# Kernel optimization log

Hardware: AMD Instinct MI355X
Metric: run time of the kernel (lower is better)

The kernel has to match this reference:

```python
import jax, jax.numpy as jnp
import numpy as np

N_NODES = 100000
N_EDGES = 3200000
IN_C, HID, OUT_C = 128, 256, 128
N_GRAPHS = 64
EPS = 1e-5


def setup_inputs() -> dict:
    key = jax.random.key(0)
    ks = jax.random.split(key, 16)
    x = jax.random.normal(ks[0], (N_NODES, IN_C), dtype=jnp.float32)
    edge_index = jax.random.randint(ks[1], (2, N_EDGES), 0, N_NODES, dtype=jnp.int64 if jax.config.jax_enable_x64 else jnp.int32)
    batch = jnp.sort(jax.random.randint(ks[2], (N_NODES,), 0, N_GRAPHS, dtype=jnp.int32))
    def glorot(k, shape):
        lim = jnp.sqrt(6.0 / (shape[-2] + shape[-1]))
        return jax.random.uniform(k, shape, jnp.float32, -lim, lim)
    return {
        "x": x,
        "W_in": glorot(ks[3], (IN_C, HID)),
        "b_in": jnp.zeros((HID,), jnp.float32),
        "g_in": jnp.ones((HID,), jnp.float32),
        "be_in": jnp.zeros((HID,), jnp.float32),
        "W_hid": glorot(ks[4], (2, HID, HID)),
        "b_hid": jnp.zeros((2, HID), jnp.float32),
        "g_hid": jnp.ones((2, HID), jnp.float32),
        "be_hid": jnp.zeros((2, HID), jnp.float32),
        "W_out": glorot(ks[5], (HID, OUT_C)),
        "b_out": jnp.zeros((OUT_C,), jnp.float32),
        "g_out": jnp.ones((OUT_C,), jnp.float32),
        "be_out": jnp.zeros((OUT_C,), jnp.float32),
        "edge_index": edge_index,
        "batch": batch,
    }


def _gcn_norm(edge_index, n_nodes):
    # add self-loops, symmetric deg^-1/2 normalization (PyG GCNConv defaults)
    loop = jnp.arange(n_nodes, dtype=edge_index.dtype)
    src = jnp.concatenate([edge_index[0], loop])
    dst = jnp.concatenate([edge_index[1], loop])
    deg = jax.ops.segment_sum(jnp.ones_like(dst, dtype=jnp.float32), dst, num_segments=n_nodes)
    dinv = jnp.where(deg > 0, jax.lax.rsqrt(deg), 0.0)
    norm = dinv[src] * dinv[dst]  # [E+N]
    return src, dst, norm


def _block(x, W, b, g, be, src, dst, norm, n_nodes):
    h = x @ W  # [N, out]
    agg = jax.ops.segment_sum(h[src] * norm[:, None], dst, num_segments=n_nodes) + b
    a = jax.nn.leaky_relu(agg, negative_slope=0.01)
    mu = jnp.mean(a, axis=0)
    var = jnp.mean(jnp.square(a - mu), axis=0)
    return (a - mu) * jax.lax.rsqrt(var + EPS) * g + be


def reference(x, W_in, b_in, g_in, be_in, W_hid, b_hid, g_hid, be_hid,
              W_out, b_out, g_out, be_out, edge_index, batch):
    n = x.shape[0]
    src, dst, norm = _gcn_norm(edge_index, n)
    h = _block(x, W_in, b_in, g_in, be_in, src, dst, norm, n)
    for i in range(W_hid.shape[0]):
        h = _block(h, W_hid[i], b_hid[i], g_hid[i], be_hid[i], src, dst, norm, n)
    h = _block(h, W_out, b_out, g_out, be_out, src, dst, norm, n)
    # global mean pool over graphs
    sums = jax.ops.segment_sum(h, batch, num_segments=N_GRAPHS)
    cnts = jax.ops.segment_sum(jnp.ones((n,), h.dtype), batch, num_segments=N_GRAPHS)
    return sums / jnp.maximum(cnts, 1.0)[:, None]
```

## Files before the change

### kernel.cpp

```cpp
#include <hip/hip_runtime.h>
#include <stdint.h>

#define EPS_LN 1e-5f

typedef short bf16x8 __attribute__((ext_vector_type(8)));
typedef float f32x4  __attribute__((ext_vector_type(4)));

__device__ __forceinline__ unsigned short f2bf(float f) {
    unsigned u = __float_as_uint(f);
    unsigned r = (u + 0x7fffu + ((u >> 16) & 1u)) >> 16;
    return (unsigned short)r;
}
__device__ __forceinline__ float bf_lo(unsigned u) { return __uint_as_float(u << 16); }
__device__ __forceinline__ float bf_hi(unsigned u) { return __uint_as_float(u & 0xffff0000u); }

__device__ __forceinline__ void async16(void* lds, const void* g) {
    __builtin_amdgcn_global_load_lds(
        (const __attribute__((address_space(1))) unsigned int*)g,
        (__attribute__((address_space(3))) unsigned int*)lds, 16, 0, 0);
}


__global__ void count_deg_kernel(const int* __restrict__ dst, int E, unsigned* __restrict__ deg) {
    int e = blockIdx.x * blockDim.x + threadIdx.x;
    if (e < E) atomicAdd(&deg[dst[e]], 1u);
}

__global__ void block_sums_kernel(const unsigned* __restrict__ deg, unsigned* __restrict__ part, int N) {
    __shared__ unsigned s[256];
    int t = threadIdx.x;
    int i0 = blockIdx.x * 512 + t * 2;
    unsigned a = (i0 < N) ? deg[i0] : 0u;
    unsigned b = (i0 + 1 < N) ? deg[i0 + 1] : 0u;
    s[t] = a + b;
    __syncthreads();
    for (int off = 128; off > 0; off >>= 1) {
        if (t < off) s[t] += s[t + off];
        __syncthreads();
    }
    if (t == 0) part[blockIdx.x] = s[0];
}

__global__ void scan_part_kernel(unsigned* __restrict__ part, unsigned* __restrict__ row_ptr,
                                 int NB, int N) {
    __shared__ unsigned s[256];
    int t = threadIdx.x;
    unsigned v = (t < NB) ? part[t] : 0u;
    s[t] = v;
    __syncthreads();
    for (int off = 1; off < 256; off <<= 1) {
        unsigned u = (t >= off) ? s[t - off] : 0u;
        __syncthreads();
        s[t] += u;
        __syncthreads();
    }
    if (t < NB) part[t] = s[t] - v;
    if (t == 255) row_ptr[N] = s[255];
}

__global__ void scan_blocks_kernel(const unsigned* __restrict__ deg, const unsigned* __restrict__ part,
                                   unsigned* __restrict__ row_ptr, unsigned* __restrict__ cursor,
                                   float* __restrict__ dinv, int N) {
    __shared__ unsigned s[256];
    int t = threadIdx.x;
    int i0 = blockIdx.x * 512 + t * 2;
    unsigned a = (i0 < N) ? deg[i0] : 0u;
    unsigned b = (i0 + 1 < N) ? deg[i0 + 1] : 0u;
    unsigned pair = a + b;
    s[t] = pair;
    __syncthreads();
    for (int off = 1; off < 256; off <<= 1) {
        unsigned u = (t >= off) ? s[t - off] : 0u;
        __syncthreads();
        s[t] += u;
        __syncthreads();
    }
    unsigned excl = s[t] - pair + part[blockIdx.x];
    if (i0 < N) {
        row_ptr[i0] = excl; cursor[i0] = excl;
        dinv[i0] = rsqrtf((float)(a + 1u));
    }
    if (i0 + 1 < N) {
        row_ptr[i0 + 1] = excl + a; cursor[i0 + 1] = excl + a;
        dinv[i0 + 1] = rsqrtf((float)(b + 1u));
    }
}

__global__ void fill_csr_kernel(const int* __restrict__ src, const int* __restrict__ dst,
                                const float* __restrict__ dinv, int E,
                                unsigned* __restrict__ cursor, uint2* __restrict__ csr) {
    int e = blockIdx.x * blockDim.x + threadIdx.x;
    if (e < E) {
        int d = dst[e];
        int s = src[e];
        unsigned pos = atomicAdd(&cursor[d], 1u);
        float w = dinv[d] * dinv[s];
        csr[pos] = make_uint2((unsigned)s, __float_as_uint(w));
    }
}

__global__ void prep_all_kernel(const float* __restrict__ x, unsigned* __restrict__ xbf,
                                const float* __restrict__ W_in, unsigned short* __restrict__ Wt_in,
                                const float* __restrict__ W_hid, unsigned short* __restrict__ Wt_h0,
                                unsigned short* __restrict__ Wt_h1, int n2) {
    int i = blockIdx.x * blockDim.x + threadIdx.x;
    if (i < n2) {
        float2 v = *reinterpret_cast<const float2*>(&x[(size_t)i * 2]);
        xbf[i] = (unsigned)f2bf(v.x) | ((unsigned)f2bf(v.y) << 16);
        return;
    }
    int r = i - n2;
    if (r < 32768) {
        int k = r >> 8, c = r & 255;
        Wt_in[(size_t)c * 128 + k] = f2bf(W_in[r]);
    } else if (r < 32768 + 65536) {
        r -= 32768;
        int k = r >> 8, c = r & 255;
        Wt_h0[(size_t)c * 256 + k] = f2bf(W_hid[r]);
    } else if (r < 32768 + 131072) {
        r -= 32768 + 65536;
        int k = r >> 8, c = r & 255;
        Wt_h1[(size_t)c * 256 + k] = f2bf(W_hid[65536 + r]);
    }
}

template<int UPL, bool AFF, bool FINAL>
__global__ void aggregate_bf(const unsigned* __restrict__ X, void* __restrict__ outp,
                             const unsigned* __restrict__ row_ptr, const uint2* __restrict__ csr,
                             const float* __restrict__ dinv,
                             const float* __restrict__ ssum, const float* __restrict__ ssq,
                             const float* __restrict__ gg, const float* __restrict__ be, float invN,
                             const float* __restrict__ tW, const float* __restrict__ bias, int N) {
    constexpr int C = UPL * 64;
    constexpr unsigned RSU = C / 2;
    constexpr int PC = UPL * 2;

    __shared__ float sL[AFF ? C : 1], tL[AFF ? C : 1];
    if constexpr (AFF) {
        for (int i = threadIdx.x; i < C; i += 256) {
            float mu = ssum[i] * invN;
            float var = ssq[i] * invN - mu * mu;
            float s = gg[i] * rsqrtf(var + EPS_LN);
            sL[i] = s;
            tL[i] = be[i] - mu * s;
        }
        __syncthreads();
    }

    int node = blockIdx.x * 8 + (threadIdx.x >> 5);
    if (node >= N) return;
    int ll = threadIdx.x & 31;
    unsigned cu = (unsigned)ll * UPL;

    float di = dinv[node];
    float w0 = di * di;
    float acc[PC];
    float wsum = w0;
    {
        const unsigned* xr = X + (size_t)((unsigned)node * RSU + cu);
        if constexpr (UPL == 4) {
            uint4 v = *reinterpret_cast<const uint4*>(xr);
            unsigned uu[4] = {v.x, v.y, v.z, v.w};
            #pragma unroll
            for (int q = 0; q < 4; ++q) {
                acc[q * 2 + 0] = w0 * bf_lo(uu[q]);
                acc[q * 2 + 1] = w0 * bf_hi(uu[q]);
            }
        } else {
            uint2 v = *reinterpret_cast<const uint2*>(xr);
            acc[0] = w0 * bf_lo(v.x); acc[1] = w0 * bf_hi(v.x);
            acc[2] = w0 * bf_lo(v.y); acc[3] = w0 * bf_hi(v.y);
        }
    }
    unsigned e0 = row_ptr[node];
    unsigned e1 = row_ptr[node + 1];
    unsigned cnt = e1 - e0;
    unsigned full = cnt & ~7u;

    for (unsigned i = 0; i < full; i += 8) {
        uint2 p[8];
        #pragma unroll
        for (int u = 0; u < 8; ++u) p[u] = csr[e0 + i + u];
        if constexpr (UPL == 4) {
            uint4 v[8];
            #pragma unroll
            for (int u = 0; u < 8; ++u)
                v[u] = *reinterpret_cast<const uint4*>(X + (size_t)(p[u].x * RSU + cu));
            #pragma unroll
            for (int u = 0; u < 8; ++u) {
                float f = __uint_as_float(p[u].y);
                unsigned uu[4] = {v[u].x, v[u].y, v[u].z, v[u].w};
                #pragma unroll
                for (int q = 0; q < 4; ++q) {
                    acc[q * 2 + 0] += f * bf_lo(uu[q]);
                    acc[q * 2 + 1] += f * bf_hi(uu[q]);
                }
                wsum += f;
            }
        } else {
            uint2 v[8];
            #pragma unroll
            for (int u = 0; u < 8; ++u)
                v[u] = *reinterpret_cast<const uint2*>(X + (size_t)(p[u].x * RSU + cu));
            #pragma unroll
            for (int u = 0; u < 8; ++u) {
                float f = __uint_as_float(p[u].y);
                acc[0] += f * bf_lo(v[u].x); acc[1] += f * bf_hi(v[u].x);
                acc[2] += f * bf_lo(v[u].y); acc[3] += f * bf_hi(v[u].y);
                wsum += f;
            }
        }
    }
    for (unsigned i = full; i < cnt; ++i) {
        uint2 p = csr[e0 + i];
        float f = __uint_as_float(p.y);
        if constexpr (UPL == 4) {
            uint4 v = *reinterpret_cast<const uint4*>(X + (size_t)(p.x * RSU + cu));
            unsigned uu[4] = {v.x, v.y, v.z, v.w};
            #pragma unroll
            for (int q = 0; q < 4; ++q) {
                acc[q * 2 + 0] += f * bf_lo(uu[q]);
                acc[q * 2 + 1] += f * bf_hi(uu[q]);
            }
        } else {
            uint2 v = *reinterpret_cast<const uint2*>(X + (size_t)(p.x * RSU + cu));
            acc[0] += f * bf_lo(v.x); acc[1] += f * bf_hi(v.x);
            acc[2] += f * bf_lo(v.y); acc[3] += f * bf_hi(v.y);
        }
        wsum += f;
    }

    int col = ll * PC;
    float z[PC];
    #pragma unroll
    for (int j = 0; j < PC; ++j) {
        float f = acc[j];
        if constexpr (AFF) f = sL[col + j] * f + tL[col + j] * wsum;
        if constexpr (FINAL) {
            f = f + wsum * tW[col + j] + bias[col + j];
            f = f > 0.f ? f : 0.01f * f;
        }
        z[j] = f;
    }
    if constexpr (FINAL) {
        float* of = (float*)outp;
        *reinterpret_cast<float4*>(&of[(size_t)node * C + col]) = make_float4(z[0], z[1], z[2], z[3]);
    } else {
        unsigned* ou = (unsigned*)outp;
        if constexpr (UPL == 4) {
            uint4 pk;
            pk.x = (unsigned)f2bf(z[0]) | ((unsigned)f2bf(z[1]) << 16);
            pk.y = (unsigned)f2bf(z[2]) | ((unsigned)f2bf(z[3]) << 16);
            pk.z = (unsigned)f2bf(z[4]) | ((unsigned)f2bf(z[5]) << 16);
            pk.w = (unsigned)f2bf(z[6]) | ((unsigned)f2bf(z[7]) << 16);
            *reinterpret_cast<uint4*>(&ou[(size_t)((unsigned)node * RSU + cu)]) = pk;
        } else {
            uint2 pk;
            pk.x = (unsigned)f2bf(z[0]) | ((unsigned)f2bf(z[1]) << 16);
            pk.y = (unsigned)f2bf(z[2]) | ((unsigned)f2bf(z[3]) << 16);
            *reinterpret_cast<uint2*>(&ou[(size_t)((unsigned)node * RSU + cu)]) = pk;
        }
    }
}

template<int K, int NN, bool EPI>
__launch_bounds__(256)
__global__ void gemm_mfma(const unsigned short* __restrict__ Z, const unsigned short* __restrict__ Wt,
                          const float* __restrict__ bias, unsigned short* __restrict__ out,
                          float* __restrict__ stat_sum, float* __restrict__ stat_sq, int M) {
    __shared__ char smem[32768];
    __shared__ float csum[128], csq[128];

    const int tid = threadIdx.x;
    const int lane = tid & 63;
    const int w = tid >> 6;
    const int wr = (w >> 1) * 64;
    const int wc = (w & 1) * 64;
    const int rowBase = blockIdx.x * 128;
    const int colBase = blockIdx.y * 128;
    const int frow = lane & 15;
    const int kgrp = lane >> 4;

    f32x4 acc[4][4] = {};

    for (int kt = 0; kt < K / 64; ++kt) {
        #pragma unroll
        for (int i = 0; i < 4; ++i) {
            int g = (i * 4 + w) * 64 + lane;
            int r = g >> 3;
            int bl = (g & 7) * 16;
            int bg = bl ^ ((r & 7) << 4);
            const char* src = (const char*)Z + (((size_t)(rowBase + r) * K + kt * 64) << 1) + bg;
            async16(&smem[(i * 4 + w) * 1024], src);
        }
        #pragma unroll
        for (int i = 0; i < 4; ++i) {
            int g = (i * 4 + w) * 64 + lane;
            int r = g >> 3;
            int bl = (g & 7) * 16;
            int bg = bl ^ ((r & 7) << 4);
            const char* src = (const char*)Wt + (((size_t)(colBase + r) * K + kt * 64) << 1) + bg;
            async16(&smem[16384 + (i * 4 + w) * 1024], src);
        }
        __syncthreads();
        #pragma unroll
        for (int kk = 0; kk < 2; ++kk) {
            const int kbyte = kk * 64 + kgrp * 16;
            bf16x8 af[4], bfr[4];
            #pragma unroll
            for (int m = 0; m < 4; ++m) {
                int r = wr + m * 16 + frow;
                af[m] = *reinterpret_cast<const bf16x8*>(&smem[r * 128 + (kbyte ^ ((r & 7) << 4))]);
            }
            #pragma unroll
            for (int n = 0; n < 4; ++n) {
                int c = wc + n * 16 + frow;
                bfr[n] = *reinterpret_cast<const bf16x8*>(&smem[16384 + c * 128 + (kbyte ^ ((c & 7) << 4))]);
            }
            #pragma unroll
            for (int m = 0; m < 4; ++m)
                #pragma unroll
                for (int n = 0; n < 4; ++n)
                    acc[m][n] = __builtin_amdgcn_mfma_f32_16x16x32_bf16(bfr[n], af[m], acc[m][n], 0, 0, 0);
        }
        __syncthreads();
    }

    if constexpr (EPI) {
        if (tid < 128) { csum[tid] = 0.f; csq[tid] = 0.f; }
        __syncthreads();
    }

    #pragma unroll
    for (int n = 0; n < 4; ++n) {
        const int c_local = wc + n * 16 + kgrp * 4;
        const int col = colBase + c_local;
        float4 b4 = make_float4(0.f, 0.f, 0.f, 0.f);
        if constexpr (EPI) b4 = *reinterpret_cast<const float4*>(&bias[col]);
        float ps[4] = {0.f, 0.f, 0.f, 0.f}, pq[4] = {0.f, 0.f, 0.f, 0.f};
        #pragma unroll
        for (int m = 0; m < 4; ++m) {
            int row = rowBase + wr + m * 16 + frow;
            if (row < M) {
                float f0 = acc[m][n][0] + b4.x;
                float f1 = acc[m][n][1] + b4.y;
                float f2 = acc[m][n][2] + b4.z;
                float f3 = acc[m][n][3] + b4.w;
                if constexpr (EPI) {
                    f0 = f0 > 0.f ? f0 : 0.01f * f0;
                    f1 = f1 > 0.f ? f1 : 0.01f * f1;
                    f2 = f2 > 0.f ? f2 : 0.01f * f2;
                    f3 = f3 > 0.f ? f3 : 0.01f * f3;
                }
                uint2 pk;
                pk.x = (unsigned)f2bf(f0) | ((unsigned)f2bf(f1) << 16);
                pk.y = (unsigned)f2bf(f2) | ((unsigned)f2bf(f3) << 16);
                *reinterpret_cast<uint2*>(&out[(size_t)row * NN + col]) = pk;
                if constexpr (EPI) {
                    ps[0] += f0; ps[1] += f1; ps[2] += f2; ps[3] += f3;
                    pq[0] += f0 * f0; pq[1] += f1 * f1; pq[2] += f2 * f2; pq[3] += f3 * f3;
                }
            }
        }
        if constexpr (EPI) {
            #pragma unroll
            for (int s = 1; s < 16; s <<= 1) {
                #pragma unroll
                for (int j = 0; j < 4; ++j) {
                    ps[j] += __shfl_xor(ps[j], s);
                    pq[j] += __shfl_xor(pq[j], s);
                }
            }
            if (frow == 0) {
                #pragma unroll
                for (int j = 0; j < 4; ++j) {
                    atomicAdd(&csum[c_local + j], ps[j]);
                    atomicAdd(&csq[c_local + j], pq[j]);
                }
            }
        }
    }
    if constexpr (EPI) {
        __syncthreads();
        if (tid < 128) {
            atomicAdd(&stat_sum[colBase + tid], csum[tid]);
            atomicAdd(&stat_sq[colBase + tid], csq[tid]);
        }
    }
}

__global__ void prep_wout_tw(const float* __restrict__ W,
                             const float* __restrict__ ssum, const float* __restrict__ ssq,
                             const float* __restrict__ gg, const float* __restrict__ be, float invN,
                             unsigned short* __restrict__ Wt, float* __restrict__ tW) {
    if (blockIdx.x < 128) {
        int idx = blockIdx.x * 256 + threadIdx.x;
        int k = idx >> 7, c = idx & 127;
        float mu = ssum[k] * invN;
        float var = ssq[k] * invN - mu * mu;
        float s = gg[k] * rsqrtf(var + EPS_LN);
        Wt[(size_t)c * 256 + k] = f2bf(s * W[idx]);
    } else {
        int c = threadIdx.x;
        if (c < 128) {
            float acc = 0.f;
            for (int k = 0; k < 256; ++k) {
                float mu = ssum[k] * invN;
                float var = ssq[k] * invN - mu * mu;
                float s = gg[k] * rsqrtf(var + EPS_LN);
                float t = be[k] - mu * s;
                acc += t * W[k * 128 + c];
            }
            tW[c] = acc;
        }
    }
}

__global__ void stats_pool_kernel(const float* __restrict__ A, const int* __restrict__ batch,
                                  float* __restrict__ stat_sum, float* __restrict__ stat_sq,
                                  float* __restrict__ psums, float* __restrict__ pcnt, int N) {
    int c = threadIdx.x;
    int n0 = blockIdx.x * 256;
    if (n0 >= N) return;
    int n1 = min(n0 + 256, N);
    float cs = 0.f, cq = 0.f;
    float acc = 0.f, cacc = 0.f;
    int curg = -1;
    for (int n = n0; n < n1; ++n) {
        float v = A[(size_t)n * 128 + c];
        cs += v; cq += v * v;
        int g = batch[n];
        if (g != curg) {
            if (curg >= 0) {
                atomicAdd(&psums[curg * 128 + c], acc);
                if (c == 0) atomicAdd(&pcnt[curg], cacc);
            }
            acc = 0.f; cacc = 0.f; curg = g;
        }
        acc += v;
        cacc += 1.f;
    }
    if (curg >= 0) {
        atomicAdd(&psums[curg * 128 + c], acc);
        if (c == 0) atomicAdd(&pcnt[curg], cacc);
    }
    atomicAdd(&stat_sum[c], cs);
    atomicAdd(&stat_sq[c], cq);
}

__global__ void divide_kernel(const float* __restrict__ psums, const float* __restrict__ pcnt,
                              const float* __restrict__ ssum, const float* __restrict__ ssq,
                              const float* __restrict__ gg, const float* __restrict__ be, float invN,
                              float* __restrict__ out) {
    int i = blockIdx.x * blockDim.x + threadIdx.x;
    if (i < 64 * 128) {
        int g = i >> 7, c = i & 127;
        float mu = ssum[c] * invN;
        float var = ssq[c] * invN - mu * mu;
        float s = gg[c] * rsqrtf(var + EPS_LN);
        float t = be[c] - mu * s;
        float cnt = pcnt[g];
        out[i] = (cnt > 0.f) ? s * (psums[i] / cnt) + t : 0.f;
    }
}

extern "C" void kernel_launch(void* const* d_in, const int* in_sizes, int n_in,
                              void* d_out, int out_size, void* d_ws, size_t ws_size,
                              hipStream_t stream) {
    const float* x      = (const float*)d_in[0];
    const float* W_in   = (const float*)d_in[1];
    const float* b_in   = (const float*)d_in[2];
    const float* g_in   = (const float*)d_in[3];
    const float* be_in  = (const float*)d_in[4];
    const float* W_hid  = (const float*)d_in[5];
    const float* b_hid  = (const float*)d_in[6];
    const float* g_hid  = (const float*)d_in[7];
    const float* be_hid = (const float*)d_in[8];
    const float* W_out  = (const float*)d_in[9];
    const float* b_out  = (const float*)d_in[10];
    const float* g_out  = (const float*)d_in[11];
    const float* be_out = (const float*)d_in[12];
    const int*   eidx   = (const int*)d_in[13];
    const int*   batch  = (const int*)d_in[14];
    float* out = (float*)d_out;

    const int N = in_sizes[14];
    const int E = in_sizes[13] / 2;
    const int Npad = ((N + 127) / 128) * 128;
    const int NB = (N + 511) / 512;
    const int* e_src = eidx;
    const int* e_dst = eidx + E;

    char* ws = (char*)d_ws;
    size_t off = 0;
    auto alloc = [&](size_t bytes) -> void* {
        void* p = ws + off;
        off = (off + bytes + 255) & ~(size_t)255;
        return p;
    };
    char* B1 = (char*)alloc((size_t)Npad * 256 * 2);
    char* B2 = (char*)alloc((size_t)Npad * 256 * 2);
    unsigned* deg      = (unsigned*)alloc((size_t)N * 4);
    float*    dinv     = (float*)alloc((size_t)N * 4);
    unsigned* row_ptr  = (unsigned*)alloc((size_t)(N + 1) * 4);
    unsigned* cursor   = (unsigned*)alloc((size_t)N * 4);
    unsigned* part     = (unsigned*)alloc(256 * 4);
    uint2*    csr      = (uint2*)alloc((size_t)E * 8);
    unsigned short* Wt_in  = (unsigned short*)alloc(256 * 128 * 2);
    unsigned short* Wt_h0  = (unsigned short*)alloc(256 * 256 * 2);
    unsigned short* Wt_h1  = (unsigned short*)alloc(256 * 256 * 2);
    unsigned short* Wt_out = (unsigned short*)alloc(128 * 256 * 2);
    float*    tW       = (float*)alloc(128 * 4);
    float*    stats    = (float*)alloc(4 * 512 * 4);
    float*    psums    = (float*)alloc(64 * 128 * 4);
    float*    pcnt     = (float*)alloc(64 * 4);

    float* s1 = stats + 0 * 512, *q1 = s1 + 256;
    float* s2 = stats + 1 * 512, *q2 = s2 + 256;
    float* s3 = stats + 2 * 512, *q3 = s3 + 256;
    float* s4 = stats + 3 * 512, *q4 = s4 + 256;

    const float invN = 1.0f / (float)N;

    hipMemsetAsync(deg, 0, (size_t)N * 4, stream);
    hipMemsetAsync(stats, 0, ((char*)pcnt + 64 * 4) - (char*)stats, stream);

    int egrid = (E + 255) / 256;
    count_deg_kernel<<<egrid, 256, 0, stream>>>(e_dst, E, deg);
    block_sums_kernel<<<NB, 256, 0, stream>>>(deg, part, N);
    scan_part_kernel<<<1, 256, 0, stream>>>(part, row_ptr, NB, N);
    scan_blocks_kernel<<<NB, 256, 0, stream>>>(deg, part, row_ptr, cursor, dinv, N);
    fill_csr_kernel<<<egrid, 256, 0, stream>>>(e_src, e_dst, dinv, E, cursor, csr);

    {
        int total = N * 64 + 32768 + 65536 + 65536;
        prep_all_kernel<<<(total + 255) / 256, 256, 0, stream>>>(
            x, (unsigned*)B2, W_in, Wt_in, W_hid, Wt_h0, Wt_h1, N * 64);
    }

    const int aggGrid = (N + 7) / 8;
    dim3 gg256(Npad / 128, 2);

    aggregate_bf<2, false, false><<<aggGrid, 256, 0, stream>>>(
        (const unsigned*)B2, B1, row_ptr, csr, dinv,
        nullptr, nullptr, nullptr, nullptr, invN, nullptr, nullptr, N);
    gemm_mfma<128, 256, true><<<gg256, 256, 0, stream>>>(
        (const unsigned short*)B1, Wt_in, b_in, (unsigned short*)B2, s1, q1, N);

    aggregate_bf<4, true, false><<<aggGrid, 256, 0, stream>>>(
        (const unsigned*)B2, B1, row_ptr, csr, dinv,
        s1, q1, g_in, be_in, invN, nullptr, nullptr, N);
    gemm_mfma<256, 256, true><<<gg256, 256, 0, stream>>>(
        (const unsigned short*)B1, Wt_h0, b_hid, (unsigned short*)B2, s2, q2, N);

    aggregate_bf<4, true, false><<<aggGrid, 256, 0, stream>>>(
        (const unsigned*)B2, B1, row_ptr, csr, dinv,
        s2, q2, g_hid, be_hid, invN, nullptr, nullptr, N);
    gemm_mfma<256, 256, true><<<gg256, 256, 0, stream>>>(
        (const unsigned short*)B1, Wt_h1, b_hid + 256, (unsigned short*)B2, s3, q3, N);

    prep_wout_tw<<<129, 256, 0, stream>>>(W_out, s3, q3, g_hid + 256, be_hid + 256, invN, Wt_out, tW);
    gemm_mfma<256, 128, false><<<dim3(Npad / 128, 1), 256, 0, stream>>>(
        (const unsigned short*)B2, Wt_out, nullptr, (unsigned short*)B1, nullptr, nullptr, N);
    aggregate_bf<2, false, true><<<aggGrid, 256, 0, stream>>>(
        (const unsigned*)B1, B2, row_ptr, csr, dinv,
        nullptr, nullptr, nullptr, nullptr, invN, tW, b_out, N);

    stats_pool_kernel<<<(N + 255) / 256, 128, 0, stream>>>(
        (const float*)B2, batch, s4, q4, psums, pcnt, N);
    divide_kernel<<<(64 * 128 + 255) / 256, 256, 0, stream>>>(
        psums, pcnt, s4, q4, g_out, be_out, invN, out);
}
```

Before: 1.314 ms.

## Fuse neighbor aggregation with MFMA GEMM and stats epilogue per 16-row tile

```diff
diff --git a/kernel.cpp b/kernel.cpp
--- a/kernel.cpp
+++ b/kernel.cpp
@@ -124,28 +124,228 @@
     }
 }
 
+template<int K, int NN, bool AFF>
+__launch_bounds__(512, 4)
+__global__ void fused_aggemm(const unsigned* __restrict__ X, const unsigned short* __restrict__ Wt,
+                             const float* __restrict__ bias,
+                             const float* __restrict__ ssum, const float* __restrict__ ssq,
+                             const float* __restrict__ gg, const float* __restrict__ be, float invN,
+                             unsigned short* __restrict__ out,
+                             const unsigned* __restrict__ row_ptr, const uint2* __restrict__ csr,
+                             const float* __restrict__ dinv,
+                             float* __restrict__ stat_sum, float* __restrict__ stat_sq, int N) {
+    constexpr int UPL = K / 64;
+    constexpr int PC  = UPL * 2;
+    constexpr unsigned RSU = K / 2;
+
+    __shared__ char atile[16 * K * 2];
+    __shared__ float sL[AFF ? K : 1], tL[AFF ? K : 1];
+    __shared__ float csum[NN], csq[NN];
+
+    const int tid = threadIdx.x;
+
+    if constexpr (AFF) {
+        for (int i = tid; i < K; i += 512) {
+            float mu = ssum[i] * invN;
+            float var = ssq[i] * invN - mu * mu;
+            float s = gg[i] * rsqrtf(var + EPS_LN);
+            sL[i] = s; tL[i] = be[i] - mu * s;
+        }
+    }
+    for (int i = tid; i < NN; i += 512) { csum[i] = 0.f; csq[i] = 0.f; }
+    __syncthreads();
+
+    const int rrow = tid >> 5;
+    const int ll = tid & 31;
+    const int node = blockIdx.x * 16 + rrow;
+    const unsigned cu = (unsigned)ll * UPL;
+
+    float acc[PC];
+    #pragma unroll
+    for (int j = 0; j < PC; ++j) acc[j] = 0.f;
+    float wsum = 0.f;
+
+    if (node < N) {
+        float di = dinv[node];
+        float w0 = di * di;
+        wsum = w0;
+        {
+            const unsigned* xr = X + (size_t)((unsigned)node * RSU + cu);
+            if constexpr (UPL == 4) {
+                uint4 v = *reinterpret_cast<const uint4*>(xr);
+                unsigned uu[4] = {v.x, v.y, v.z, v.w};
+                #pragma unroll
+                for (int q = 0; q < 4; ++q) {
+                    acc[q * 2 + 0] = w0 * bf_lo(uu[q]);
+                    acc[q * 2 + 1] = w0 * bf_hi(uu[q]);
+                }
+            } else {
+                uint2 v = *reinterpret_cast<const uint2*>(xr);
+                acc[0] = w0 * bf_lo(v.x); acc[1] = w0 * bf_hi(v.x);
+                acc[2] = w0 * bf_lo(v.y); acc[3] = w0 * bf_hi(v.y);
+            }
+        }
+        unsigned e0 = row_ptr[node];
+        unsigned e1 = row_ptr[node + 1];
+        unsigned cnt = e1 - e0;
+        unsigned full = cnt & ~7u;
+
+        for (unsigned i = 0; i < full; i += 8) {
+            uint2 p[8];
+            #pragma unroll
+            for (int u = 0; u < 8; ++u) p[u] = csr[e0 + i + u];
+            if constexpr (UPL == 4) {
+                uint4 v[8];
+                #pragma unroll
+                for (int u = 0; u < 8; ++u)
+                    v[u] = *reinterpret_cast<const uint4*>(X + (size_t)(p[u].x * RSU + cu));
+                #pragma unroll
+                for (int u = 0; u < 8; ++u) {
+                    float f = __uint_as_float(p[u].y);
+                    unsigned uu[4] = {v[u].x, v[u].y, v[u].z, v[u].w};
+                    #pragma unroll
+                    for (int q = 0; q < 4; ++q) {
+                        acc[q * 2 + 0] += f * bf_lo(uu[q]);
+                        acc[q * 2 + 1] += f * bf_hi(uu[q]);
+                    }
+                    wsum += f;
+                }
+            } else {
+                uint2 v[8];
+                #pragma unroll
+                for (int u = 0; u < 8; ++u)
+                    v[u] = *reinterpret_cast<const uint2*>(X + (size_t)(p[u].x * RSU + cu));
+                #pragma unroll
+                for (int u = 0; u < 8; ++u) {
+                    float f = __uint_as_float(p[u].y);
+                    acc[0] += f * bf_lo(v[u].x); acc[1] += f * bf_hi(v[u].x);
+                    acc[2] += f * bf_lo(v[u].y); acc[3] += f * bf_hi(v[u].y);
+                    wsum += f;
+                }
+            }
+        }
+        for (unsigned i = full; i < cnt; ++i) {
+            uint2 p = csr[e0 + i];
+            float f = __uint_as_float(p.y);
+            if constexpr (UPL == 4) {
+                uint4 v = *reinterpret_cast<const uint4*>(X + (size_t)(p.x * RSU + cu));
+                unsigned uu[4] = {v.x, v.y, v.z, v.w};
+                #pragma unroll
+                for (int q = 0; q < 4; ++q) {
+                    acc[q * 2 + 0] += f * bf_lo(uu[q]);
+                    acc[q * 2 + 1] += f * bf_hi(uu[q]);
+                }
+            } else {
+                uint2 v = *reinterpret_cast<const uint2*>(X + (size_t)(p.x * RSU + cu));
+                acc[0] += f * bf_lo(v.x); acc[1] += f * bf_hi(v.x);
+                acc[2] += f * bf_lo(v.y); acc[3] += f * bf_hi(v.y);
+            }
+            wsum += f;
+        }
+
+        if constexpr (AFF) {
+            int col = ll * PC;
+            #pragma unroll
+            for (int j = 0; j < PC; ++j)
+                acc[j] = sL[col + j] * acc[j] + tL[col + j] * wsum;
+        }
+    }
+
+    {
+        char* myrow = atile + rrow * (K * 2);
+        if constexpr (UPL == 4) {
+            uint4 pk;
+            pk.x = (unsigned)f2bf(acc[0]) | ((unsigned)f2bf(acc[1]) << 16);
+            pk.y = (unsigned)f2bf(acc[2]) | ((unsigned)f2bf(acc[3]) << 16);
+            pk.z = (unsigned)f2bf(acc[4]) | ((unsigned)f2bf(acc[5]) << 16);
+            pk.w = (unsigned)f2bf(acc[6]) | ((unsigned)f2bf(acc[7]) << 16);
+            int off = (ll * 16) ^ ((rrow & 7) << 4);
+            *reinterpret_cast<uint4*>(myrow + off) = pk;
+        } else {
+            uint2 pk;
+            pk.x = (unsigned)f2bf(acc[0]) | ((unsigned)f2bf(acc[1]) << 16);
+            pk.y = (unsigned)f2bf(acc[2]) | ((unsigned)f2bf(acc[3]) << 16);
+            int off = (ll * 8) ^ ((rrow & 7) << 4);
+            *reinterpret_cast<uint2*>(myrow + off) = pk;
+        }
+    }
+    __syncthreads();
+
+    const int w = tid >> 6;
+    const int lane = tid & 63;
+    const int frow = lane & 15;
+    const int kgrp = lane >> 4;
+    f32x4 macc[2] = {};
+
+    #pragma unroll
+    for (int kt = 0; kt < K / 32; ++kt) {
+        int aoff = frow * (K * 2) + ((kt * 64 + kgrp * 16) ^ ((frow & 7) << 4));
+        bf16x8 af = *reinterpret_cast<const bf16x8*>(atile + aoff);
+        #pragma unroll
+        for (int n = 0; n < 2; ++n) {
+            int c = w * 32 + n * 16 + frow;
+            bf16x8 bfr = *reinterpret_cast<const bf16x8*>(Wt + (size_t)c * K + kt * 32 + kgrp * 8);
+            macc[n] = __builtin_amdgcn_mfma_f32_16x16x32_bf16(bfr, af, macc[n], 0, 0, 0);
+        }
+    }
+
+    const int orow = blockIdx.x * 16 + frow;
+    const bool rok = orow < N;
+    #pragma unroll
+    for (int n = 0; n < 2; ++n) {
+        const int c0 = w * 32 + n * 16 + kgrp * 4;
+        float4 b4 = *reinterpret_cast<const float4*>(&bias[c0]);
+        float f0 = macc[n][0] + b4.x;
+        float f1 = macc[n][1] + b4.y;
+        float f2 = macc[n][2] + b4.z;
+        float f3 = macc[n][3] + b4.w;
+        f0 = f0 > 0.f ? f0 : 0.01f * f0;
+        f1 = f1 > 0.f ? f1 : 0.01f * f1;
+        f2 = f2 > 0.f ? f2 : 0.01f * f2;
+        f3 = f3 > 0.f ? f3 : 0.01f * f3;
+        float ps[4], pq[4];
+        if (rok) {
+            uint2 pk;
+            pk.x = (unsigned)f2bf(f0) | ((unsigned)f2bf(f1) << 16);
+            pk.y = (unsigned)f2bf(f2) | ((unsigned)f2bf(f3) << 16);
+            *reinterpret_cast<uint2*>(&out[(size_t)orow * NN + c0]) = pk;
+            ps[0] = f0; ps[1] = f1; ps[2] = f2; ps[3] = f3;
+            pq[0] = f0 * f0; pq[1] = f1 * f1; pq[2] = f2 * f2; pq[3] = f3 * f3;
+        } else {
+            ps[0] = ps[1] = ps[2] = ps[3] = 0.f;
+            pq[0] = pq[1] = pq[2] = pq[3] = 0.f;
+        }
+        #pragma unroll
+        for (int s = 1; s < 16; s <<= 1) {
+            #pragma unroll
+            for (int j = 0; j < 4; ++j) {
+                ps[j] += __shfl_xor(ps[j], s);
+                pq[j] += __shfl_xor(pq[j], s);
+            }
+        }
+        if (frow == 0) {
+            #pragma unroll
+            for (int j = 0; j < 4; ++j) {
+                atomicAdd(&csum[c0 + j], ps[j]);
+                atomicAdd(&csq[c0 + j], pq[j]);
+            }
+        }
+    }
+    __syncthreads();
+    for (int i = tid; i < NN; i += 512) {
+        atomicAdd(&stat_sum[i], csum[i]);
+        atomicAdd(&stat_sq[i], csq[i]);
+    }
+}
+
 template<int UPL, bool AFF, bool FINAL>
 __global__ void aggregate_bf(const unsigned* __restrict__ X, void* __restrict__ outp,
                              const unsigned* __restrict__ row_ptr, const uint2* __restrict__ csr,
                              const float* __restrict__ dinv,
-                             const float* __restrict__ ssum, const float* __restrict__ ssq,
-                             const float* __restrict__ gg, const float* __restrict__ be, float invN,
                              const float* __restrict__ tW, const float* __restrict__ bias, int N) {
     constexpr int C = UPL * 64;
     constexpr unsigned RSU = C / 2;
     constexpr int PC = UPL * 2;
-
-    __shared__ float sL[AFF ? C : 1], tL[AFF ? C : 1];
-    if constexpr (AFF) {
-        for (int i = threadIdx.x; i < C; i += 256) {
-            float mu = ssum[i] * invN;
-            float var = ssq[i] * invN - mu * mu;
-            float s = gg[i] * rsqrtf(var + EPS_LN);
-            sL[i] = s;
-            tL[i] = be[i] - mu * s;
-        }
-        __syncthreads();
-    }
 
     int node = blockIdx.x * 8 + (threadIdx.x >> 5);
     if (node >= N) return;
@@ -158,19 +358,9 @@
     float wsum = w0;
     {
         const unsigned* xr = X + (size_t)((unsigned)node * RSU + cu);
-        if constexpr (UPL == 4) {
-            uint4 v = *reinterpret_cast<const uint4*>(xr);
-            unsigned uu[4] = {v.x, v.y, v.z, v.w};
-            #pragma unroll
-            for (int q = 0; q < 4; ++q) {
-                acc[q * 2 + 0] = w0 * bf_lo(uu[q]);
-                acc[q * 2 + 1] = w0 * bf_hi(uu[q]);
-            }
-        } else {
-            uint2 v = *reinterpret_cast<const uint2*>(xr);
-            acc[0] = w0 * bf_lo(v.x); acc[1] = w0 * bf_hi(v.x);
-            acc[2] = w0 * bf_lo(v.y); acc[3] = w0 * bf_hi(v.y);
-        }
+        uint2 v = *reinterpret_cast<const uint2*>(xr);
+        acc[0] = w0 * bf_lo(v.x); acc[1] = w0 * bf_hi(v.x);
+        acc[2] = w0 * bf_lo(v.y); acc[3] = w0 * bf_hi(v.y);
     }
     unsigned e0 = row_ptr[node];
     unsigned e1 = row_ptr[node + 1];
@@ -181,52 +371,24 @@
         uint2 p[8];
         #pragma unroll
         for (int u = 0; u < 8; ++u) p[u] = csr[e0 + i + u];
-        if constexpr (UPL == 4) {
-            uint4 v[8];
-            #pragma unroll
-            for (int u = 0; u < 8; ++u)
-                v[u] = *reinterpret_cast<const uint4*>(X + (size_t)(p[u].x * RSU + cu));
-            #pragma unroll
-            for (int u = 0; u < 8; ++u) {
-                float f = __uint_as_float(p[u].y);
-                unsigned uu[4] = {v[u].x, v[u].y, v[u].z, v[u].w};
-                #pragma unroll
-                for (int q = 0; q < 4; ++q) {
-                    acc[q * 2 + 0] += f * bf_lo(uu[q]);
-                    acc[q * 2 + 1] += f * bf_hi(uu[q]);
-                }
-                wsum += f;
-            }
-        } else {
-            uint2 v[8];
-            #pragma unroll
-            for (int u = 0; u < 8; ++u)
-                v[u] = *reinterpret_cast<const uint2*>(X + (size_t)(p[u].x * RSU + cu));
-            #pragma unroll
-            for (int u = 0; u < 8; ++u) {
-                float f = __uint_as_float(p[u].y);
-                acc[0] += f * bf_lo(v[u].x); acc[1] += f * bf_hi(v[u].x);
-                acc[2] += f * bf_lo(v[u].y); acc[3] += f * bf_hi(v[u].y);
-                wsum += f;
-            }
+        uint2 v[8];
+        #pragma unroll
+        for (int u = 0; u < 8; ++u)
+            v[u] = *reinterpret_cast<const uint2*>(X + (size_t)(p[u].x * RSU + cu));
+        #pragma unroll
+        for (int u = 0; u < 8; ++u) {
+            float f = __uint_as_float(p[u].y);
+            acc[0] += f * bf_lo(v[u].x); acc[1] += f * bf_hi(v[u].x);
+            acc[2] += f * bf_lo(v[u].y); acc[3] += f * bf_hi(v[u].y);
+            wsum += f;
         }
     }
     for (unsigned i = full; i < cnt; ++i) {
         uint2 p = csr[e0 + i];
+        uint2 v = *reinterpret_cast<const uint2*>(X + (size_t)(p.x * RSU + cu));
         float f = __uint_as_float(p.y);
-        if constexpr (UPL == 4) {
-            uint4 v = *reinterpret_cast<const uint4*>(X + (size_t)(p.x * RSU + cu));
-            unsigned uu[4] = {v.x, v.y, v.z, v.w};
-            #pragma unroll
-            for (int q = 0; q < 4; ++q) {
-                acc[q * 2 + 0] += f * bf_lo(uu[q]);
-                acc[q * 2 + 1] += f * bf_hi(uu[q]);
-            }
-        } else {
-            uint2 v = *reinterpret_cast<const uint2*>(X + (size_t)(p.x * RSU + cu));
-            acc[0] += f * bf_lo(v.x); acc[1] += f * bf_hi(v.x);
-            acc[2] += f * bf_lo(v.y); acc[3] += f * bf_hi(v.y);
-        }
+        acc[0] += f * bf_lo(v.x); acc[1] += f * bf_hi(v.x);
+        acc[2] += f * bf_lo(v.y); acc[3] += f * bf_hi(v.y);
         wsum += f;
     }
 
@@ -235,32 +397,12 @@
     #pragma unroll
     for (int j = 0; j < PC; ++j) {
         float f = acc[j];
-        if constexpr (AFF) f = sL[col + j] * f + tL[col + j] * wsum;
-        if constexpr (FINAL) {
-            f = f + wsum * tW[col + j] + bias[col + j];
-            f = f > 0.f ? f : 0.01f * f;
-        }
+        f = f + wsum * tW[col + j] + bias[col + j];
+        f = f > 0.f ? f : 0.01f * f;
         z[j] = f;
     }
-    if constexpr (FINAL) {
-        float* of = (float*)outp;
-        *reinterpret_cast<float4*>(&of[(size_t)node * C + col]) = make_float4(z[0], z[1], z[2], z[3]);
-    } else {
-        unsigned* ou = (unsigned*)outp;
-        if constexpr (UPL == 4) {
-            uint4 pk;
-            pk.x = (unsigned)f2bf(z[0]) | ((unsigned)f2bf(z[1]) << 16);
-            pk.y = (unsigned)f2bf(z[2]) | ((unsigned)f2bf(z[3]) << 16);
-            pk.z = (unsigned)f2bf(z[4]) | ((unsigned)f2bf(z[5]) << 16);
-            pk.w = (unsigned)f2bf(z[6]) | ((unsigned)f2bf(z[7]) << 16);
-            *reinterpret_cast<uint4*>(&ou[(size_t)((unsigned)node * RSU + cu)]) = pk;
-        } else {
-            uint2 pk;
-            pk.x = (unsigned)f2bf(z[0]) | ((unsigned)f2bf(z[1]) << 16);
-            pk.y = (unsigned)f2bf(z[2]) | ((unsigned)f2bf(z[3]) << 16);
-            *reinterpret_cast<uint2*>(&ou[(size_t)((unsigned)node * RSU + cu)]) = pk;
-        }
-    }
+    float* of = (float*)outp;
+    *reinterpret_cast<float4*>(&of[(size_t)node * C + col]) = make_float4(z[0], z[1], z[2], z[3]);
 }
 
 template<int K, int NN, bool EPI>
@@ -269,7 +411,6 @@
                           const float* __restrict__ bias, unsigned short* __restrict__ out,
                           float* __restrict__ stat_sum, float* __restrict__ stat_sq, int M) {
     __shared__ char smem[32768];
-    __shared__ float csum[128], csq[128];
 
     const int tid = threadIdx.x;
     const int lane = tid & 63;
@@ -326,65 +467,19 @@
         __syncthreads();
     }
 
-    if constexpr (EPI) {
-        if (tid < 128) { csum[tid] = 0.f; csq[tid] = 0.f; }
-        __syncthreads();
-    }
-
     #pragma unroll
     for (int n = 0; n < 4; ++n) {
         const int c_local = wc + n * 16 + kgrp * 4;
         const int col = colBase + c_local;
-        float4 b4 = make_float4(0.f, 0.f, 0.f, 0.f);
-        if constexpr (EPI) b4 = *reinterpret_cast<const float4*>(&bias[col]);
-        float ps[4] = {0.f, 0.f, 0.f, 0.f}, pq[4] = {0.f, 0.f, 0.f, 0.f};
         #pragma unroll
         for (int m = 0; m < 4; ++m) {
             int row = rowBase + wr + m * 16 + frow;
             if (row < M) {
-                float f0 = acc[m][n][0] + b4.x;
-                float f1 = acc[m][n][1] + b4.y;
-                float f2 = acc[m][n][2] + b4.z;
-                float f3 = acc[m][n][3] + b4.w;
-                if constexpr (EPI) {
-                    f0 = f0 > 0.f ? f0 : 0.01f * f0;
-                    f1 = f1 > 0.f ? f1 : 0.01f * f1;
-                    f2 = f2 > 0.f ? f2 : 0.01f * f2;
-                    f3 = f3 > 0.f ? f3 : 0.01f * f3;
-                }
                 uint2 pk;
-                pk.x = (unsigned)f2bf(f0) | ((unsigned)f2bf(f1) << 16);
-                pk.y = (unsigned)f2bf(f2) | ((unsigned)f2bf(f3) << 16);
+                pk.x = (unsigned)f2bf(acc[m][n][0]) | ((unsigned)f2bf(acc[m][n][1]) << 16);
+                pk.y = (unsigned)f2bf(acc[m][n][2]) | ((unsigned)f2bf(acc[m][n][3]) << 16);
                 *reinterpret_cast<uint2*>(&out[(size_t)row * NN + col]) = pk;
-                if constexpr (EPI) {
-                    ps[0] += f0; ps[1] += f1; ps[2] += f2; ps[3] += f3;
-                    pq[0] += f0 * f0; pq[1] += f1 * f1; pq[2] += f2 * f2; pq[3] += f3 * f3;
-                }
-            }
-        }
-        if constexpr (EPI) {
-            #pragma unroll
-            for (int s = 1; s < 16; s <<= 1) {
-                #pragma unroll
-                for (int j = 0; j < 4; ++j) {
-                    ps[j] += __shfl_xor(ps[j], s);
-                    pq[j] += __shfl_xor(pq[j], s);
-                }
-            }
-            if (frow == 0) {
-                #pragma unroll
-                for (int j = 0; j < 4; ++j) {
-                    atomicAdd(&csum[c_local + j], ps[j]);
-                    atomicAdd(&csq[c_local + j], pq[j]);
-                }
-            }
-        }
-    }
-    if constexpr (EPI) {
-        __syncthreads();
-        if (tid < 128) {
-            atomicAdd(&stat_sum[colBase + tid], csum[tid]);
-            atomicAdd(&stat_sq[colBase + tid], csq[tid]);
+            }
         }
     }
 }
@@ -538,36 +633,28 @@
             x, (unsigned*)B2, W_in, Wt_in, W_hid, Wt_h0, Wt_h1, N * 64);
     }
 
-    const int aggGrid = (N + 7) / 8;
-    dim3 gg256(Npad / 128, 2);
-
-    aggregate_bf<2, false, false><<<aggGrid, 256, 0, stream>>>(
-        (const unsigned*)B2, B1, row_ptr, csr, dinv,
-        nullptr, nullptr, nullptr, nullptr, invN, nullptr, nullptr, N);
-    gemm_mfma<128, 256, true><<<gg256, 256, 0, stream>>>(
-        (const unsigned short*)B1, Wt_in, b_in, (unsigned short*)B2, s1, q1, N);
-
-    aggregate_bf<4, true, false><<<aggGrid, 256, 0, stream>>>(
-        (const unsigned*)B2, B1, row_ptr, csr, dinv,
-        s1, q1, g_in, be_in, invN, nullptr, nullptr, N);
-    gemm_mfma<256, 256, true><<<gg256, 256, 0, stream>>>(
-        (const unsigned short*)B1, Wt_h0, b_hid, (unsigned short*)B2, s2, q2, N);
-
-    aggregate_bf<4, true, false><<<aggGrid, 256, 0, stream>>>(
-        (const unsigned*)B2, B1, row_ptr, csr, dinv,
-        s2, q2, g_hid, be_hid, invN, nullptr, nullptr, N);
-    gemm_mfma<256, 256, true><<<gg256, 256, 0, stream>>>(
-        (const unsigned short*)B1, Wt_h1, b_hid + 256, (unsigned short*)B2, s3, q3, N);
+    const int fusedGrid = (N + 15) / 16;
+
+    fused_aggemm<128, 256, false><<<fusedGrid, 512, 0, stream>>>(
+        (const unsigned*)B2, Wt_in, b_in, nullptr, nullptr, nullptr, nullptr, invN,
+        (unsigned short*)B1, row_ptr, csr, dinv, s1, q1, N);
+
+    fused_aggemm<256, 256, true><<<fusedGrid, 512, 0, stream>>>(
+        (const unsigned*)B1, Wt_h0, b_hid, s1, q1, g_in, be_in, invN,
+        (unsigned short*)B2, row_ptr, csr, dinv, s2, q2, N);
+
+    fused_aggemm<256, 256, true><<<fusedGrid, 512, 0, stream>>>(
+        (const unsigned*)B2, Wt_h1, b_hid + 256, s2, q2, g_hid, be_hid, invN,
+        (unsigned short*)B1, row_ptr, csr, dinv, s3, q3, N);
 
     prep_wout_tw<<<129, 256, 0, stream>>>(W_out, s3, q3, g_hid + 256, be_hid + 256, invN, Wt_out, tW);
     gemm_mfma<256, 128, false><<<dim3(Npad / 128, 1), 256, 0, stream>>>(
-        (const unsigned short*)B2, Wt_out, nullptr, (unsigned short*)B1, nullptr, nullptr, N);
-    aggregate_bf<2, false, true><<<aggGrid, 256, 0, stream>>>(
-        (const unsigned*)B1, B2, row_ptr, csr, dinv,
-        nullptr, nullptr, nullptr, nullptr, invN, tW, b_out, N);
+        (const unsigned short*)B1, Wt_out, nullptr, (unsigned short*)B2, nullptr, nullptr, N);
+    aggregate_bf<2, false, true><<<(N + 7) / 8, 256, 0, stream>>>(
+        (const unsigned*)B2, B1, row_ptr, csr, dinv, tW, b_out, N);
 
     stats_pool_kernel<<<(N + 255) / 256, 128, 0, stream>>>(
-        (const float*)B2, batch, s4, q4, psums, pcnt, N);
+        (const float*)B1, batch, s4, q4, psums, pcnt, N);
     divide_kernel<<<(64 * 128 + 255) / 256, 256, 0, stream>>>(
         psums, pcnt, s4, q4, g_out, be_out, invN, out);
 }
```

Result: slower. 1.466 ms (+11.6%).
